# Optimization experiments

Hardware: AMD Instinct MI355X
Metric: run time of the kernel (lower is better)

Reference implementation:

```python
import jax, jax.numpy as jnp
import numpy as np

LAM = 0.01   # sparsity_threshold -> softshrink lambda
EPS = 1e-8

def _ln(x, g, b):
    mu = jnp.mean(x, axis=-1, keepdims=True)
    var = jnp.mean((x - mu) ** 2, axis=-1, keepdims=True)
    return (x - mu) / jnp.sqrt(var + 1e-5) * g + b

def _cmatmul(xr, xi, w, b):
    # x: (B,H,W,nb,i)  w: (2,nb,i,o)  b: (2,nb,o)  -> complex block-diagonal matmul
    o_r = jnp.einsum('bhwni,nio->bhwno', xr, w[0]) - jnp.einsum('bhwni,nio->bhwno', xi, w[1]) + b[0]
    o_i = jnp.einsum('bhwni,nio->bhwno', xi, w[0]) + jnp.einsum('bhwni,nio->bhwno', xr, w[1]) + b[1]
    return o_r, o_i

def _softshrink(v):
    return jnp.where(v > LAM, v - LAM, jnp.where(v < -LAM, v + LAM, 0.0))

def _afno(xn, xp, w1, b1, w2, b2, w3, b3, alpha, H, W):
    # xn: (B,N,C_in) tokens, xp: (B,H,W,hid). layer_i == 0 path, num_blocks == 1.
    B, N, C = xn.shape
    hid = alpha.shape[-1]
    xf = jnp.fft.fft2(xn.reshape(B, H, W, C), axes=(1, 2), norm='ortho')
    xr = xf.real.reshape(B, H, W, 1, C)
    xi = xf.imag.reshape(B, H, W, 1, C)
    o1r, o1i = _cmatmul(xr, xi, w1, b1)           # (B,H,W,1,hid)
    xr = o1r.reshape(B, H, W, hid)
    xi = o1i.reshape(B, H, W, hid)
    pf = jnp.fft.fft2(xp, axes=(1, 2), norm='ortho')
    pr = pf.real.reshape(B, H, W, 1, hid)
    pi = pf.imag.reshape(B, H, W, 1, hid)
    tr, ti = _cmatmul(pr, pi, w3, b3)
    pr = tr.reshape(B, H, W, hid)
    pi = ti.reshape(B, H, W, hid)
    # Pangu-guided frequency modulation (real/imag component form)
    cross_r = pr * xr + pi * xi                   # Re(x_pangu * conj(x))
    mag_o = jnp.sqrt(xr ** 2 + xi ** 2)
    mag_p = jnp.sqrt(pr ** 2 + pi ** 2)
    phi_x = jnp.arctan2(xi, xr)
    phi_p = jnp.arctan2(pi, pr)
    sum_cos = alpha * jnp.cos(phi_x) + (1.0 - alpha) * jnp.cos(phi_p)
    sum_sin = alpha * jnp.sin(phi_x) + (1.0 - alpha) * jnp.sin(phi_p)
    nrm = jnp.sqrt(sum_cos ** 2 + sum_sin ** 2 + EPS)
    out_cos = sum_cos / nrm
    out_sin = sum_sin / nrm
    sim = cross_r / (mag_p * mag_o + EPS)
    soft = jax.nn.softmax(sim, axis=3)
    mag = mag_o * soft
    o1r = jax.nn.relu(mag * out_cos).reshape(B, H, W, 1, hid)
    o1i = jax.nn.relu(mag * out_sin).reshape(B, H, W, 1, hid)
    o2r, o2i = _cmatmul(o1r, o1i, w2, b2)
    o2r = _softshrink(o2r)
    o2i = _softshrink(o2i)
    xc = jax.lax.complex(o2r.reshape(B, H, W, hid), o2i.reshape(B, H, W, hid))
    y = jnp.fft.ifft2(xc, s=(H, W), axes=(1, 2), norm='ortho').real
    return y.reshape(B, N, hid)

def reference(x, x_pangu, z_fft, w1, b1, w2, b2, w3, b3, alpha,
              gamma1, beta1, gamma2, beta2, proj_w, proj_b,
              fc1_w, fc1_b, fc2_w, fc2_b):
    B, C, H, W = x.shape
    tok = x.reshape(B, C, H * W).transpose(0, 2, 1)      # (B,N,C_in)
    xp = x_pangu.transpose(0, 2, 3, 1)                   # (B,H,W,hid)
    residual = tok @ proj_w.T + proj_b                   # C_in != dim -> proj
    f = _afno(_ln(tok, gamma1, beta1), xp, w1, b1, w2, b2, w3, b3, alpha, H, W)
    h = f + residual                                     # double skip
    m = _ln(h, gamma2, beta2)
    m = jax.nn.gelu(m @ fc1_w.T + fc1_b, approximate=False) @ fc2_w.T + fc2_b
    out = m + h
    return out.reshape(B, H, W, -1).transpose(0, 3, 1, 2)

def setup_inputs():
    key = jax.random.key(0)
    ks = jax.random.split(key, 12)
    B, Cin, H, W = 8, 128, 64, 64
    hid, nb, mlp_hid = 256, 1, 2048
    s = 0.02
    return {
        'x': jax.random.normal(ks[0], (B, Cin, H, W), jnp.float32),
        'x_pangu': jax.random.normal(ks[1], (B, hid, H, W), jnp.float32),
        'z_fft': jax.random.normal(ks[2], (B, H, W, hid, 2), jnp.float32),
        'w1': s * jax.random.normal(ks[3], (2, nb, Cin, hid), jnp.float32),
        'b1': s * jax.random.normal(ks[4], (2, nb, hid), jnp.float32),
        'w2': s * jax.random.normal(ks[5], (2, nb, hid, hid), jnp.float32),
        'b2': s * jax.random.normal(ks[6], (2, nb, hid), jnp.float32),
        'w3': s * jax.random.normal(ks[7], (2, nb, hid, hid), jnp.float32),
        'b3': s * jax.random.normal(ks[8], (2, nb, hid), jnp.float32),
        'alpha': jnp.full((1, 1, 1, hid), 0.5, jnp.float32),
        'gamma1': jnp.ones((Cin,), jnp.float32),
        'beta1': jnp.zeros((Cin,), jnp.float32),
        'gamma2': jnp.ones((hid,), jnp.float32),
        'beta2': jnp.zeros((hid,), jnp.float32),
        'proj_w': s * jax.random.normal(ks[9], (hid, Cin), jnp.float32),
        'proj_b': jnp.zeros((hid,), jnp.float32),
        'fc1_w': s * jax.random.normal(ks[10], (mlp_hid, hid), jnp.float32),
        'fc1_b': jnp.zeros((mlp_hid,), jnp.float32),
        'fc2_w': s * jax.random.normal(ks[11], (hid, mlp_hid), jnp.float32),
        'fc2_b': jnp.zeros((hid,), jnp.float32),
    }
```

## Files before the change

kernel.cpp:

```cpp
#include <hip/hip_runtime.h>
#include <hip/hip_bf16.h>
#include <math.h>

#define NBATCH 8
#define HWP 4096
#define NTOK 32768
#define NTOKH 16896
#define CIN 128
#define HID 256
#define MLPH 2048
#define SLOTF 8388608L

typedef unsigned short u16;
typedef __attribute__((ext_vector_type(8))) short bf16x8;
typedef __attribute__((ext_vector_type(4))) float f32x4;
typedef __attribute__((ext_vector_type(8))) unsigned short ushort8_t;
typedef __attribute__((ext_vector_type(2))) unsigned long long u64x2;

__device__ __forceinline__ float bf2f(u16 v) { return __uint_as_float(((unsigned)v) << 16); }
__device__ __forceinline__ u16 f2bf(float f) {
    unsigned u = __float_as_uint(f);
    u = u + 0x7fffu + ((u >> 16) & 1u);
    return (u16)(u >> 16);
}
__device__ __forceinline__ u16 bits2bf(unsigned u) {
    u = u + 0x7fffu + ((u >> 16) & 1u);
    return (u16)(u >> 16);
}
__device__ __forceinline__ unsigned pk_bf16(float lo, float hi) {
    unsigned r;
    asm("v_cvt_pk_bf16_f32 %0, %1, %2" : "=v"(r) : "v"(lo), "v"(hi));
    return r;
}
__device__ __forceinline__ float sshrink(float v) {
    return v > 0.01f ? v - 0.01f : (v < -0.01f ? v + 0.01f : 0.f);
}
__device__ __forceinline__ float fast_gelu(float v) {
    float z = v * fmaf(0.0713548162726f, v * v, 1.59576912161f);
    float t = __builtin_amdgcn_exp2f(z * -1.44269504088896f);
    return v * __builtin_amdgcn_rcpf(1.f + t);
}

__global__ __launch_bounds__(256) void ln1_kernel(const float* __restrict__ x,
    const float* __restrict__ g, const float* __restrict__ be,
    u16* __restrict__ xnb, u16* __restrict__ xb)
{
    __shared__ float xt[CIN][65];
    __shared__ float mu_s[64], rs_s[64];
    int bid = blockIdx.x;
    int b = bid >> 6;
    int t0 = (bid & 63) << 6;
    int tid = threadIdx.x;
    for (int it = 0; it < 32; ++it) {
        int idx = (it << 8) + tid;
        int c = idx >> 6, t = idx & 63;
        xt[c][t] = x[(long)(b * CIN + c) * HWP + t0 + t];
    }
    __syncthreads();
    int tt = tid >> 2, p = tid & 3;
    float s = 0.f, ss = 0.f;
    #pragma unroll
    for (int i = 0; i < 32; ++i) {
        float v = xt[p * 32 + i][tt];
        s += v; ss += v * v;
    }
    s += __shfl_xor(s, 1); ss += __shfl_xor(ss, 1);
    s += __shfl_xor(s, 2); ss += __shfl_xor(ss, 2);
    if (p == 0) {
        float mu = s * (1.f / CIN);
        float var = ss * (1.f / CIN) - mu * mu;
        mu_s[tt] = mu;
        rs_s[tt] = rsqrtf(var + 1e-5f);
    }
    __syncthreads();
    #pragma unroll
    for (int it = 0; it < 16; ++it) {
        int idx = (it << 8) + tid;
        int t = idx >> 6, c2 = (idx & 63) << 1;
        float v0 = (xt[c2][t] - mu_s[t]) * rs_s[t] * g[c2] + be[c2];
        float v1 = (xt[c2 + 1][t] - mu_s[t]) * rs_s[t] * g[c2 + 1] + be[c2 + 1];
        *(unsigned*)&xnb[((long)b * HWP + t0 + t) * CIN + c2] = pk_bf16(v0, v1);
    }
    #pragma unroll
    for (int it = 0; it < 8; ++it) {
        int idx = (it << 8) + tid;
        int t = idx >> 5, c4 = (idx & 31) << 2;
        uint2 pk;
        pk.x = pk_bf16(xt[c4 + 0][t], xt[c4 + 1][t]);
        pk.y = pk_bf16(xt[c4 + 2][t], xt[c4 + 3][t]);
        *(uint2*)&xb[((long)b * HWP + t0 + t) * CIN + c4] = pk;
    }
}

__device__ __forceinline__ void wcvt_body(const float* __restrict__ w, int K,
    u16* __restrict__ out, int idx)
{
    int k = idx >> 8, o = idx & 255;
    float w0 = w[k * 256 + o];
    float w1v = w[K * 256 + k * 256 + o];
    long K2 = 2L * K;
    out[(long)o * K2 + k] = f2bf(w0);
    out[(long)o * K2 + K + k] = f2bf(-w1v);
    out[(long)(256 + o) * K2 + k] = f2bf(w1v);
    out[(long)(256 + o) * K2 + K + k] = f2bf(w0);
}
__device__ __forceinline__ void f2bf_body(const float* __restrict__ in,
    u16* __restrict__ out, int i)
{
    float4 v = *(const float4*)&in[i];
    ushort4 o;
    o.x = f2bf(v.x); o.y = f2bf(v.y); o.z = f2bf(v.z); o.w = f2bf(v.w);
    *(ushort4*)&out[i] = o;
}
__global__ __launch_bounds__(256) void setup_kernel(
    const float* __restrict__ w1, const float* __restrict__ w3,
    const float* __restrict__ w2, const float* __restrict__ fc1w,
    const float* __restrict__ fc2w, const float* __restrict__ pw,
    u16* __restrict__ TWB, u16* __restrict__ W1c, u16* __restrict__ W3c,
    u16* __restrict__ W2c, u16* __restrict__ WB1, u16* __restrict__ WB2,
    u16* __restrict__ PWB)
{
    int bid = blockIdx.x, tid = threadIdx.x;
    if (bid < 64) {
        int idx = bid * 256 + tid;
        int n = idx >> 7, kcol = idx & 127;
        int j = kcol & 63, p = kcol >> 6;
        int np = n & 63, q = n >> 6;
        float th = 6.283185307179586f * (float)((j * np) & 63) / 64.f;
        float sv, cv;
        sincosf(th, &sv, &cv);
        float fw = (q == 0) ? (p == 0 ? cv : sv) : (p == 0 ? -sv : cv);
        float iv = (q == 0) ? (p == 0 ? cv : -sv) : (p == 0 ? sv : cv);
        fw *= 0.125f; iv *= 0.125f;
        u16 fh = f2bf(fw), ih = f2bf(iv);
        TWB[idx] = fh;
        TWB[16384 + idx] = f2bf(fw - bf2f(fh));
        TWB[32768 + idx] = ih;
        TWB[49152 + idx] = f2bf(iv - bf2f(ih));
    } else if (bid < 192) {
        wcvt_body(w1, 128, W1c, (bid - 64) * 256 + tid);
    } else if (bid < 448) {
        wcvt_body(w3, 256, W3c, (bid - 192) * 256 + tid);
    } else if (bid < 704) {
        wcvt_body(w2, 256, W2c, (bid - 448) * 256 + tid);
    } else if (bid < 1216) {
        f2bf_body(fc1w, WB1, ((bid - 704) * 256 + tid) * 4);
    } else if (bid < 1728) {
        f2bf_body(fc2w, WB2, ((bid - 1216) * 256 + tid) * 4);
    } else {
        f2bf_body(pw, PWB, ((bid - 1728) * 256 + tid) * 4);
    }
}

template<int INMODE, int REALOUT, int NT, int USELO>
__global__ __launch_bounds__(256) void dftm_kernel(
    const void* __restrict__ inp, const u16* __restrict__ tw,
    void* __restrict__ outp, const float* __restrict__ addend,
    int nch, long IB, long IK, long IC, long JS, long PS,
    long OB, long OK, long OC, long KS, long PS2, int kmax)
{
    constexpr int K = (INMODE == 1) ? 128 : 64;
    constexpr int AST = (K == 128) ? 136 : 72;
    constexpr int MFR = REALOUT ? 2 : 4;
    __shared__ __align__(16) u16 smem[128 * 136];
    int tid = threadIdx.x;
    int lane = tid & 63;
    int bid = blockIdx.x;
    int b = bid / (64 * nch);
    int rem = bid % (64 * nch);
    int keep = rem / nch;
    int ch = rem % nch;
    long ibase = b * IB + keep * IK + ch * IC;
    long obase = b * OB + keep * OK + ch * OC;

    if (INMODE == 0) {
        const float* inF = (const float*)inp;
        #pragma unroll
        for (int it = 0; it < 8; ++it) {
            int idx = (it << 8) + tid;
            int j = idx >> 5, c4 = (idx & 31) << 2;
            u64x2 v = *(const u64x2*)(inF + ibase + (long)j * JS + c4);
            #pragma unroll
            for (int i = 0; i < 4; ++i) {
                int vv = (i + lane) & 3;
                unsigned long long q = (vv & 2) ? v.y : v.x;
                unsigned fb = (unsigned)(q >> ((vv & 1) << 5));
                smem[(c4 + vv) * AST + j] = bits2bf(fb);
            }
        }
    } else if (INMODE == 1) {
        const u16* inU = (const u16*)inp;
        #pragma unroll
        for (int it = 0; it < 8; ++it) {
            int idx = (it << 8) + tid;
            int run = idx >> 4, c8 = (idx & 15) << 3;
            int j = run >> 1, p = run & 1;
            u64x2 v = *(const u64x2*)(inU + ibase + (long)j * JS + (long)p * PS + c8);
            int col = p * 64 + j;
            #pragma unroll
            for (int i = 0; i < 8; ++i) {
                int vv = (i + lane) & 7;
                unsigned long long q = (vv & 4) ? v.y : v.x;
                u16 val = (u16)(q >> ((vv & 3) << 4));
                smem[(c8 + vv) * AST + col] = val;
            }
        }
    } else if (INMODE == 3) {
        const u16* inU = (const u16*)inp;
        #pragma unroll
        for (int it = 0; it < 4; ++it) {
            int idx = (it << 8) + tid;
            int j = idx >> 4, c8 = (idx & 15) << 3;
            u64x2 v = *(const u64x2*)(inU + ibase + (long)j * JS + c8);
            #pragma unroll
            for (int i = 0; i < 8; ++i) {
                int vv = (i + lane) & 7;
                unsigned long long q = (vv & 4) ? v.y : v.x;
                u16 val = (u16)(q >> ((vv & 3) << 4));
                smem[(c8 + vv) * AST + j] = val;
            }
        }
    } else {
        const float* inF = (const float*)inp;
        #pragma unroll
        for (int it = 0; it < 8; ++it) {
            int idx = (it << 8) + tid;
            int row = idx >> 4, j4 = (idx & 15) << 2;
            u64x2 v = *(const u64x2*)(inF + ibase + (long)row * JS + j4);
            ushort4 o;
            o.x = bits2bf((unsigned)v.x);
            o.y = bits2bf((unsigned)(v.x >> 32));
            o.z = bits2bf((unsigned)v.y);
            o.w = bits2bf((unsigned)(v.y >> 32));
            *(ushort4*)&smem[row * AST + j4] = o;
        }
    }
    __syncthreads();

    int w = tid >> 6;
    int ln15 = lane & 15, kg = lane >> 4;
    int wrow = REALOUT ? (w << 5) : ((w >> 1) << 6);
    int wcol = REALOUT ? 0 : ((w & 1) << 6);
    f32x4 acc[MFR][NT] = {};
    #pragma unroll
    for (int kk = 0; kk < K / 32; ++kk) {
        bf16x8 av[MFR];
        #pragma unroll
        for (int m = 0; m < MFR; ++m)
            av[m] = *(const bf16x8*)&smem[(wrow + m * 16 + ln15) * AST + kk * 32 + kg * 8];
        #pragma unroll
        for (int n = 0; n < NT; ++n) {
            const u16* tb = tw + (wcol + n * 16 + ln15) * 128 + kk * 32 + kg * 8;
            bf16x8 bh = *(const bf16x8*)tb;
            #pragma unroll
            for (int m = 0; m < MFR; ++m)
                acc[m][n] = __builtin_amdgcn_mfma_f32_16x16x32_bf16(av[m], bh, acc[m][n], 0, 0, 0);
            if (USELO) {
                bf16x8 bl = *(const bf16x8*)(tb + 16384);
                #pragma unroll
                for (int m = 0; m < MFR; ++m)
                    acc[m][n] = __builtin_amdgcn_mfma_f32_16x16x32_bf16(av[m], bl, acc[m][n], 0, 0, 0);
            }
        }
    }
    __syncthreads();

    if (REALOUT == 0) {
        #pragma unroll
        for (int m = 0; m < MFR; ++m)
            #pragma unroll
            for (int n = 0; n < NT; ++n) {
                int base = (wcol + n * 16 + ln15) * 136 + wrow + m * 16 + kg * 4;
                uint2 pk;
                pk.x = pk_bf16(acc[m][n][0], acc[m][n][1]);
                pk.y = pk_bf16(acc[m][n][2], acc[m][n][3]);
                *(uint2*)&smem[base] = pk;
            }
        __syncthreads();
        u16* outU = (u16*)outp;
        #pragma unroll
        for (int it = 0; it < 8; ++it) {
            int idx = (it << 8) + tid;
            int n = idx >> 4, c8 = (idx & 15) << 3;
            int k = n & 63, p = n >> 6;
            if (k <= kmax)
                *(ushort8_t*)&outU[obase + (long)k * KS + (long)p * PS2 + c8] =
                    *(const ushort8_t*)&smem[n * 136 + c8];
        }
    } else {
        float* ef = (float*)smem;
        #pragma unroll
        for (int m = 0; m < MFR; ++m)
            #pragma unroll
            for (int n = 0; n < NT; ++n) {
                float4 vv = make_float4(acc[m][n][0], acc[m][n][1], acc[m][n][2], acc[m][n][3]);
                *(float4*)&ef[(n * 16 + ln15) * 132 + wrow + m * 16 + kg * 4] = vv;
            }
        __syncthreads();
        float* outF = (float*)outp;
        #pragma unroll
        for (int it = 0; it < 8; ++it) {
            int idx = (it << 8) + tid;
            int k = idx >> 5, c4 = (idx & 31) << 2;
            long a = obase + (long)k * KS + c4;
            float4 v = *(const float4*)&ef[k * 132 + c4];
            float4 rv = *(const float4*)&addend[a];
            v.x += rv.x; v.y += rv.y; v.z += rv.z; v.w += rv.w;
            *(float4*)&outF[a] = v;
        }
    }
}

__global__ __launch_bounds__(256) void mod_kernel(
    const u16* __restrict__ x1, const u16* __restrict__ p3,
    const float* __restrict__ alpha, u16* __restrict__ a2)
{
    int tid = threadIdx.x;
    int lane = tid & 63;
    int wv = tid >> 6;
    int tp = blockIdx.x * 4 + wv;
    int b = tp / 2112;
    int r = tp - b * 2112;
    int kh = r >> 6, kw = r & 63;
    long ibase = (long)tp * 512 + lane * 4;
    ushort4 xr4 = *(const ushort4*)&x1[ibase];
    ushort4 xi4 = *(const ushort4*)&x1[ibase + 256];
    ushort4 pr4 = *(const ushort4*)&p3[ibase];
    ushort4 pi4 = *(const ushort4*)&p3[ibase + 256];
    float4 al4 = *(const float4*)&alpha[lane * 4];
    u16 xru[4] = {xr4.x, xr4.y, xr4.z, xr4.w};
    u16 xiu[4] = {xi4.x, xi4.y, xi4.z, xi4.w};
    u16 pru[4] = {pr4.x, pr4.y, pr4.z, pr4.w};
    u16 piu[4] = {pi4.x, pi4.y, pi4.z, pi4.w};
    float alv[4] = {al4.x, al4.y, al4.z, al4.w};
    float mo[4], oc[4], os[4], sim[4];
    #pragma unroll
    for (int q = 0; q < 4; ++q) {
        float xr = bf2f(xru[q]), xi = bf2f(xiu[q]);
        float pr = bf2f(pru[q]), pi = bf2f(piu[q]);
        float al = alv[q];
        float m = __builtin_amdgcn_sqrtf(xr * xr + xi * xi);
        float mp = __builtin_amdgcn_sqrtf(pr * pr + pi * pi);
        float cx, sx, cp, sp;
        if (m > 0.f) { float rr = __builtin_amdgcn_rcpf(m); cx = xr * rr; sx = xi * rr; }
        else { cx = 1.f; sx = 0.f; }
        if (mp > 0.f) { float rr = __builtin_amdgcn_rcpf(mp); cp = pr * rr; sp = pi * rr; }
        else { cp = 1.f; sp = 0.f; }
        float sc = al * cx + (1.f - al) * cp;
        float ssn = al * sx + (1.f - al) * sp;
        float rn = __builtin_amdgcn_rsqf(sc * sc + ssn * ssn + 1e-8f);
        mo[q] = m;
        oc[q] = sc * rn;
        os[q] = ssn * rn;
        float cross = pr * xr + pi * xi;
        sim[q] = cross * __builtin_amdgcn_rcpf(mp * m + 1e-8f);
    }
    float mv = fmaxf(fmaxf(sim[0], sim[1]), fmaxf(sim[2], sim[3]));
    #pragma unroll
    for (int off = 1; off < 64; off <<= 1) mv = fmaxf(mv, __shfl_xor(mv, off));
    float e[4];
    float sum = 0.f;
    #pragma unroll
    for (int q = 0; q < 4; ++q) {
        e[q] = __builtin_amdgcn_exp2f((sim[q] - mv) * 1.44269504088896f);
        sum += e[q];
    }
    #pragma unroll
    for (int off = 1; off < 64; off <<= 1) sum += __shfl_xor(sum, off);
    float rs = __builtin_amdgcn_rcpf(sum);
    float orf[4], ipf[4], imf[4];
    #pragma unroll
    for (int q = 0; q < 4; ++q) {
        float mag = mo[q] * e[q] * rs;
        orf[q] = fmaxf(mag * oc[q], 0.f);
        ipf[q] = fmaxf(mag * os[q], 0.f);
        imf[q] = fmaxf(-mag * os[q], 0.f);
    }
    uint2 o_r, o_ip, o_im;
    o_r.x = pk_bf16(orf[0], orf[1]);  o_r.y = pk_bf16(orf[2], orf[3]);
    o_ip.x = pk_bf16(ipf[0], ipf[1]); o_ip.y = pk_bf16(ipf[2], ipf[3]);
    o_im.x = pk_bf16(imf[0], imf[1]); o_im.y = pk_bf16(imf[2], imf[3]);
    long pbase = ((long)b * 4096 + kh * 64 + kw) * 512 + lane * 4;
    *(uint2*)&a2[pbase] = o_r;
    *(uint2*)&a2[pbase + 256] = o_ip;
    if (kh >= 1 && kh <= 31) {
        long mbase = ((long)b * 4096 + (64 - kh) * 64 + ((64 - kw) & 63)) * 512 + lane * 4;
        *(uint2*)&a2[mbase] = o_r;
        *(uint2*)&a2[mbase + 256] = o_im;
    }
}

__global__ __launch_bounds__(256) void ln2_kernel(const float* __restrict__ h,
    const float* __restrict__ g, const float* __restrict__ be, u16* __restrict__ m)
{
    int t = blockIdx.x, c = threadIdx.x;
    float v = h[(long)t * HID + c];
    float s = v, ss = v * v;
    #pragma unroll
    for (int off = 1; off < 64; off <<= 1) { s += __shfl_xor(s, off); ss += __shfl_xor(ss, off); }
    __shared__ float r1[4], r2[4];
    int wid = c >> 6;
    if ((c & 63) == 0) { r1[wid] = s; r2[wid] = ss; }
    __syncthreads();
    s = r1[0] + r1[1] + r1[2] + r1[3];
    ss = r2[0] + r2[1] + r2[2] + r2[3];
    float mu = s * (1.f / HID);
    float var = ss * (1.f / HID) - mu * mu;
    float rstd = rsqrtf(var + 1e-5f);
    m[(long)t * HID + c] = f2bf((v - mu) * rstd * g[c] + be[c]);
}

template<int EPI, int BK>
__global__ __launch_bounds__(256) void gemm_mfma_kernel(
    const u16* __restrict__ A, const u16* __restrict__ Bw,
    const float* __restrict__ bias, const float* __restrict__ hbuf,
    void* __restrict__ outp, int M, int N, int K)
{
    constexpr bool SWAP = (EPI == 0 || EPI == 2 || EPI == 4);
    __shared__ __align__(16) char smem[(EPI == 1 || EPI == 5) ? (128 * 132 * 4) : (128 * 136 * 2)];
    u16* ldsA = (u16*)smem;
    u16* ldsB = (u16*)(smem + 128 * BK * 2);
    int tid = threadIdx.x;
    int nbn = N >> 7;
    int cpx = (int)gridDim.x >> 3;
    int bid = ((int)blockIdx.x & 7) * cpx + ((int)blockIdx.x >> 3);
    int bRow = (bid / nbn) << 7;
    int bCol = (bid % nbn) << 7;
    int lane = tid & 63;
    int w = tid >> 6;
    int wr = (w >> 1) << 6;
    int wc = (w & 1) << 6;
    int ln15 = lane & 15;
    int kg = lane >> 4;

    f32x4 acc[4][4] = {};

    constexpr int GR = BK / 8;
    int srow = tid / GR;
    int sg = tid % GR;
    int gsg = sg ^ (srow & 7);
    const u16* gA = A + (long)(bRow + srow) * K + gsg * 8;
    const u16* gB = Bw + (long)(bCol + srow) * K + gsg * 8;
    u16* lA = ldsA + srow * BK + sg * 8;
    u16* lB = ldsB + srow * BK + sg * 8;
    constexpr int RPR = 256 / GR;
    constexpr int NCH = 128 / RPR;

    for (int k0 = 0; k0 < K; k0 += BK) {
        __syncthreads();
        #pragma unroll
        for (int c = 0; c < NCH; ++c) {
            __builtin_amdgcn_global_load_lds(
                (const __attribute__((address_space(1))) void*)(gA + (long)c * RPR * K + k0),
                (__attribute__((address_space(3))) void*)(lA + c * RPR * BK), 16, 0, 0);
            __builtin_amdgcn_global_load_lds(
                (const __attribute__((address_space(1))) void*)(gB + (long)c * RPR * K + k0),
                (__attribute__((address_space(3))) void*)(lB + c * RPR * BK), 16, 0, 0);
        }
        __syncthreads();
        #pragma unroll
        for (int kk = 0; kk < BK; kk += 32) {
            int gbase = (kk >> 3) + kg;
            bf16x8 av[4], bv[4];
            #pragma unroll
            for (int m = 0; m < 4; ++m) {
                int row = wr + m * 16 + ln15;
                av[m] = *(const bf16x8*)(ldsA + row * BK + ((gbase ^ (row & 7)) << 3));
            }
            #pragma unroll
            for (int n = 0; n < 4; ++n) {
                int row = wc + n * 16 + ln15;
                bv[n] = *(const bf16x8*)(ldsB + row * BK + ((gbase ^ (row & 7)) << 3));
            }
            #pragma unroll
            for (int m = 0; m < 4; ++m)
                #pragma unroll
                for (int n = 0; n < 4; ++n) {
                    if (SWAP)
                        acc[m][n] = __builtin_amdgcn_mfma_f32_16x16x32_bf16(bv[n], av[m], acc[m][n], 0, 0, 0);
                    else
                        acc[m][n] = __builtin_amdgcn_mfma_f32_16x16x32_bf16(av[m], bv[n], acc[m][n], 0, 0, 0);
                }
        }
    }
    __syncthreads();

    if (EPI == 0 || EPI == 2 || EPI == 4) {
        u16* lds2 = (u16*)smem;
        #pragma unroll
        for (int n = 0; n < 4; ++n) {
            float4 bn4 = *(const float4*)&bias[bCol + wc + n * 16 + kg * 4];
            #pragma unroll
            for (int m = 0; m < 4; ++m) {
                float v0 = acc[m][n][0] + bn4.x;
                float v1 = acc[m][n][1] + bn4.y;
                float v2 = acc[m][n][2] + bn4.z;
                float v3 = acc[m][n][3] + bn4.w;
                if (EPI == 0) { v0 = fast_gelu(v0); v1 = fast_gelu(v1); v2 = fast_gelu(v2); v3 = fast_gelu(v3); }
                if (EPI == 4) { v0 = sshrink(v0); v1 = sshrink(v1); v2 = sshrink(v2); v3 = sshrink(v3); }
                uint2 pk;
                pk.x = pk_bf16(v0, v1);
                pk.y = pk_bf16(v2, v3);
                int tokenLocal = wr + m * 16 + ln15;
                int nLocal = wc + n * 16 + kg * 4;
                *(uint2*)&lds2[tokenLocal * 136 + nLocal] = pk;
            }
        }
        __syncthreads();
        u16* O = (u16*)outp;
        #pragma unroll
        for (int it = 0; it < 8; ++it) {
            int idx = (it << 8) + tid;
            int row = idx >> 4, c8 = (idx & 15) << 3;
            *(ushort8_t*)&O[(long)(bRow + row) * N + bCol + c8] = *(const ushort8_t*)&lds2[row * 136 + c8];
        }
    } else if (EPI == 5) {
        float* ldsf = (float*)smem;
        float bn[4];
        #pragma unroll
        for (int n = 0; n < 4; ++n) bn[n] = bias[bCol + wc + n * 16 + ln15];
        #pragma unroll
        for (int m = 0; m < 4; ++m)
            #pragma unroll
            for (int n = 0; n < 4; ++n) {
                int col = wc + n * 16 + ln15;
                #pragma unroll
                for (int r = 0; r < 4; ++r) {
                    int row = wr + m * 16 + kg * 4 + r;
                    ldsf[row * 132 + col] = acc[m][n][r] + bn[n];
                }
            }
        __syncthreads();
        float* O = (float*)outp;
        #pragma unroll
        for (int it = 0; it < 16; ++it) {
            int idx = (it << 8) + tid;
            int row = idx >> 5, c4 = (idx & 31) << 2;
            *(float4*)&O[(long)(bRow + row) * N + bCol + c4] = *(const float4*)&ldsf[row * 132 + c4];
        }
    } else {
        float* ldsf = (float*)smem;
        float bn[4];
        #pragma unroll
        for (int n = 0; n < 4; ++n) bn[n] = bias[bCol + wc + n * 16 + ln15];
        #pragma unroll
        for (int m = 0; m < 4; ++m)
            #pragma unroll
            for (int n = 0; n < 4; ++n) {
                int col = wc + n * 16 + ln15;
                float4 vv;
                #pragma unroll
                for (int r = 0; r < 4; ++r) {
                    int row = wr + m * 16 + kg * 4 + r;
                    float v = acc[m][n][r] + bn[n] + hbuf[(long)(bRow + row) * HID + bCol + col];
                    ((float*)&vv)[r] = v;
                }
                *(float4*)&ldsf[col * 132 + wr + m * 16 + kg * 4] = vv;
            }
        __syncthreads();
        float* O = (float*)outp;
        int b = bRow >> 12;
        int s0 = bRow & 4095;
        #pragma unroll
        for (int it = 0; it < 16; ++it) {
            int idx = (it << 8) + tid;
            int oc = idx >> 5, r4 = (idx & 31) << 2;
            *(float4*)&O[((long)(b * HID + bCol + oc)) * HWP + s0 + r4] = *(const float4*)&ldsf[oc * 132 + r4];
        }
    }
}

extern "C" void kernel_launch(void* const* d_in, const int* in_sizes, int n_in,
                              void* d_out, int out_size, void* d_ws, size_t ws_size,
                              hipStream_t stream)
{
    (void)in_sizes; (void)n_in; (void)out_size; (void)ws_size;
    const float* x     = (const float*)d_in[0];
    const float* xp    = (const float*)d_in[1];
    const float* w1    = (const float*)d_in[3];
    const float* b1    = (const float*)d_in[4];
    const float* w2    = (const float*)d_in[5];
    const float* b2    = (const float*)d_in[6];
    const float* w3    = (const float*)d_in[7];
    const float* b3    = (const float*)d_in[8];
    const float* alpha = (const float*)d_in[9];
    const float* g1    = (const float*)d_in[10];
    const float* be1   = (const float*)d_in[11];
    const float* g2    = (const float*)d_in[12];
    const float* be2   = (const float*)d_in[13];
    const float* pw    = (const float*)d_in[14];
    const float* pb    = (const float*)d_in[15];
    const float* fc1w  = (const float*)d_in[16];
    const float* fc1b  = (const float*)d_in[17];
    const float* fc2w  = (const float*)d_in[18];
    const float* fc2b  = (const float*)d_in[19];
    float* out = (float*)d_out;

    float* ws = (float*)d_ws;
    float* S0 = ws + 0 * SLOTF;
    float* S1 = ws + 1 * SLOTF;
    float* S2 = ws + 2 * SLOTF;
    float* S3 = ws + 3 * SLOTF;
    float* S4 = ws + 4 * SLOTF;
    float* S5 = ws + 5 * SLOTF;
    float* S6 = ws + 6 * SLOTF;

    float* RES  = S0;
    u16*   XNB  = (u16*)S1;
    u16*   M1x  = (u16*)S2;
    u16*   XF   = (u16*)S3;
    u16*   X1   = (u16*)S4;
    u16*   M1p  = (u16*)S2;
    u16*   PF   = (u16*)S3;
    u16*   P3   = (u16*)S5;
    u16*   A2   = (u16*)S2;
    u16*   O2b  = (u16*)S3;
    u16*   M2   = (u16*)S2;
    float* Hb   = S6;
    u16*   Mb16 = (u16*)S1;
    u16*   HIDB = (u16*)S2;

    u16* TWB  = (u16*)(S1 + SLOTF / 2);
    u16* TW_F = TWB;
    u16* TW_I = TWB + 32768;
    u16* W1c  = TWB + 65536;
    u16* W3c  = W1c + 131072;
    u16* W2c  = W3c + 262144;
    u16* WB1  = W2c + 262144;
    u16* WB2  = WB1 + 524288;
    u16* PWB  = WB2 + 524288;
    u16* XB   = TWB + 2097152;

    dim3 blk(256);

    setup_kernel<<<1760, blk, 0, stream>>>(w1, w3, w2, fc1w, fc2w, pw,
        TWB, W1c, W3c, W2c, WB1, WB2, PWB);

    ln1_kernel<<<512, blk, 0, stream>>>(x, g1, be1, XNB, XB);
    gemm_mfma_kernel<5, 128><<<512, blk, 0, stream>>>(XB, PWB, pb, nullptr,
        (void*)RES, NTOK, HID, CIN);

    dftm_kernel<3, 0, 4, 0><<<512, blk, 0, stream>>>(XNB, TW_F, M1x, nullptr,
        1, 524288L, 8192L, 0L, 128L, 0L, 1048576L, 16384L, 0L, 128L, 8192L, 63);
    dftm_kernel<1, 0, 3, 0><<<512, blk, 0, stream>>>(M1x, TW_F, XF, nullptr,
        1, 1048576L, 128L, 0L, 16384L, 8192L, 540672L, 256L, 0L, 16384L, 128L, 32);
    gemm_mfma_kernel<2, 64><<<528, blk, 0, stream>>>(XF, W1c, b1, nullptr,
        (void*)X1, NTOKH, 512, 256);

    dftm_kernel<2, 0, 4, 0><<<1024, blk, 0, stream>>>(xp, TW_F, M1p, nullptr,
        2, 1048576L, 64L, 524288L, 4096L, 0L, 2097152L, 32768L, 128L, 256L, 16384L, 63);
    dftm_kernel<1, 0, 3, 0><<<1024, blk, 0, stream>>>(M1p, TW_F, PF, nullptr,
        2, 2097152L, 256L, 128L, 32768L, 16384L, 1081344L, 512L, 128L, 32768L, 256L, 32);
    gemm_mfma_kernel<2, 64><<<528, blk, 0, stream>>>(PF, W3c, b3, nullptr,
        (void*)P3, NTOKH, 512, 512);

    mod_kernel<<<4224, blk, 0, stream>>>(X1, P3, alpha, A2);
    gemm_mfma_kernel<4, 64><<<1024, blk, 0, stream>>>(A2, W2c, b2, nullptr,
        (void*)O2b, NTOK, 512, 512);

    dftm_kernel<1, 0, 4, 0><<<1024, blk, 0, stream>>>(O2b, TW_I, M2, nullptr,
        2, 2097152L, 512L, 128L, 32768L, 256L, 2097152L, 256L, 128L, 32768L, 16384L, 63);
    dftm_kernel<1, 1, 4, 1><<<1024, blk, 0, stream>>>(M2, TW_I, Hb, RES,
        2, 2097152L, 32768L, 128L, 256L, 16384L, 1048576L, 16384L, 128L, 256L, 0L, 63);

    ln2_kernel<<<32768, blk, 0, stream>>>(Hb, g2, be2, Mb16);
    gemm_mfma_kernel<0, 64><<<4096, blk, 0, stream>>>(Mb16, WB1, fc1b, nullptr,
        (void*)HIDB, NTOK, MLPH, HID);
    gemm_mfma_kernel<1, 128><<<512, blk, 0, stream>>>(HIDB, WB2, fc2b, Hb,
        (void*)out, NTOK, HID, MLPH);
}
```

Baseline: 332.4 us.

## Double-buffer LDS tiles in MFMA GEMM to overlap global loads with compute

The GEMM kernel now uses two 64-wide K tiles in LDS and issues the global-to-LDS loads for the next tile before computing on the current one, with one barrier per iteration instead of two. BK is fixed at 64 for all GEMMs, including those that previously used 128. This aims to hide global load latency behind MFMA work. In exchange, LDS use per block grows to 64 KB, which may lower occupancy. Relying on a single barrier per iteration without an explicit vmcnt wait also risks the async LDS loads not being complete when the tile is read.

```diff
diff --git a/kernel.cpp b/kernel.cpp
--- a/kernel.cpp
+++ b/kernel.cpp
@@ -410,16 +410,14 @@
     m[(long)t * HID + c] = f2bf((v - mu) * rstd * g[c] + be[c]);
 }
 
-template<int EPI, int BK>
+template<int EPI>
 __global__ __launch_bounds__(256) void gemm_mfma_kernel(
     const u16* __restrict__ A, const u16* __restrict__ Bw,
     const float* __restrict__ bias, const float* __restrict__ hbuf,
     void* __restrict__ outp, int M, int N, int K)
 {
     constexpr bool SWAP = (EPI == 0 || EPI == 2 || EPI == 4);
-    __shared__ __align__(16) char smem[(EPI == 1 || EPI == 5) ? (128 * 132 * 4) : (128 * 136 * 2)];
-    u16* ldsA = (u16*)smem;
-    u16* ldsB = (u16*)(smem + 128 * BK * 2);
+    __shared__ __align__(16) char smem[(EPI == 1 || EPI == 5) ? (128 * 132 * 4) : 65536];
     int tid = threadIdx.x;
     int nbn = N >> 7;
     int cpx = (int)gridDim.x >> 3;
@@ -435,42 +433,60 @@
 
     f32x4 acc[4][4] = {};
 
-    constexpr int GR = BK / 8;
-    int srow = tid / GR;
-    int sg = tid % GR;
+    int srow = tid >> 3;
+    int sg = tid & 7;
     int gsg = sg ^ (srow & 7);
     const u16* gA = A + (long)(bRow + srow) * K + gsg * 8;
     const u16* gB = Bw + (long)(bCol + srow) * K + gsg * 8;
-    u16* lA = ldsA + srow * BK + sg * 8;
-    u16* lB = ldsB + srow * BK + sg * 8;
-    constexpr int RPR = 256 / GR;
-    constexpr int NCH = 128 / RPR;
-
-    for (int k0 = 0; k0 < K; k0 += BK) {
+
+    int nt = K >> 6;
+
+    {
+        u16* lA = (u16*)smem + srow * 64 + sg * 8;
+        u16* lB = (u16*)(smem + 16384) + srow * 64 + sg * 8;
+        #pragma unroll
+        for (int c = 0; c < 4; ++c) {
+            __builtin_amdgcn_global_load_lds(
+                (const __attribute__((address_space(1))) void*)(gA + (long)c * 32 * K),
+                (__attribute__((address_space(3))) void*)(lA + c * 32 * 64), 16, 0, 0);
+            __builtin_amdgcn_global_load_lds(
+                (const __attribute__((address_space(1))) void*)(gB + (long)c * 32 * K),
+                (__attribute__((address_space(3))) void*)(lB + c * 32 * 64), 16, 0, 0);
+        }
+    }
+
+    int cur = 0;
+    for (int t = 0; t < nt; ++t) {
         __syncthreads();
-        #pragma unroll
-        for (int c = 0; c < NCH; ++c) {
-            __builtin_amdgcn_global_load_lds(
-                (const __attribute__((address_space(1))) void*)(gA + (long)c * RPR * K + k0),
-                (__attribute__((address_space(3))) void*)(lA + c * RPR * BK), 16, 0, 0);
-            __builtin_amdgcn_global_load_lds(
-                (const __attribute__((address_space(1))) void*)(gB + (long)c * RPR * K + k0),
-                (__attribute__((address_space(3))) void*)(lB + c * RPR * BK), 16, 0, 0);
-        }
-        __syncthreads();
-        #pragma unroll
-        for (int kk = 0; kk < BK; kk += 32) {
+        if (t + 1 < nt) {
+            int k0 = (t + 1) << 6;
+            u16* lA = (u16*)(smem + (cur ^ 1) * 32768) + srow * 64 + sg * 8;
+            u16* lB = (u16*)(smem + (cur ^ 1) * 32768 + 16384) + srow * 64 + sg * 8;
+            #pragma unroll
+            for (int c = 0; c < 4; ++c) {
+                __builtin_amdgcn_global_load_lds(
+                    (const __attribute__((address_space(1))) void*)(gA + (long)c * 32 * K + k0),
+                    (__attribute__((address_space(3))) void*)(lA + c * 32 * 64), 16, 0, 0);
+                __builtin_amdgcn_global_load_lds(
+                    (const __attribute__((address_space(1))) void*)(gB + (long)c * 32 * K + k0),
+                    (__attribute__((address_space(3))) void*)(lB + c * 32 * 64), 16, 0, 0);
+            }
+        }
+        u16* ldsA = (u16*)(smem + cur * 32768);
+        u16* ldsB = (u16*)(smem + cur * 32768 + 16384);
+        #pragma unroll
+        for (int kk = 0; kk < 64; kk += 32) {
             int gbase = (kk >> 3) + kg;
             bf16x8 av[4], bv[4];
             #pragma unroll
             for (int m = 0; m < 4; ++m) {
                 int row = wr + m * 16 + ln15;
-                av[m] = *(const bf16x8*)(ldsA + row * BK + ((gbase ^ (row & 7)) << 3));
+                av[m] = *(const bf16x8*)(ldsA + row * 64 + ((gbase ^ (row & 7)) << 3));
             }
             #pragma unroll
             for (int n = 0; n < 4; ++n) {
                 int row = wc + n * 16 + ln15;
-                bv[n] = *(const bf16x8*)(ldsB + row * BK + ((gbase ^ (row & 7)) << 3));
+                bv[n] = *(const bf16x8*)(ldsB + row * 64 + ((gbase ^ (row & 7)) << 3));
             }
             #pragma unroll
             for (int m = 0; m < 4; ++m)
@@ -482,6 +498,7 @@
                         acc[m][n] = __builtin_amdgcn_mfma_f32_16x16x32_bf16(av[m], bv[n], acc[m][n], 0, 0, 0);
                 }
         }
+        cur ^= 1;
     }
     __syncthreads();
 
@@ -637,25 +654,25 @@
         TWB, W1c, W3c, W2c, WB1, WB2, PWB);
 
     ln1_kernel<<<512, blk, 0, stream>>>(x, g1, be1, XNB, XB);
-    gemm_mfma_kernel<5, 128><<<512, blk, 0, stream>>>(XB, PWB, pb, nullptr,
+    gemm_mfma_kernel<5><<<512, blk, 0, stream>>>(XB, PWB, pb, nullptr,
         (void*)RES, NTOK, HID, CIN);
 
     dftm_kernel<3, 0, 4, 0><<<512, blk, 0, stream>>>(XNB, TW_F, M1x, nullptr,
         1, 524288L, 8192L, 0L, 128L, 0L, 1048576L, 16384L, 0L, 128L, 8192L, 63);
     dftm_kernel<1, 0, 3, 0><<<512, blk, 0, stream>>>(M1x, TW_F, XF, nullptr,
         1, 1048576L, 128L, 0L, 16384L, 8192L, 540672L, 256L, 0L, 16384L, 128L, 32);
-    gemm_mfma_kernel<2, 64><<<528, blk, 0, stream>>>(XF, W1c, b1, nullptr,
+    gemm_mfma_kernel<2><<<528, blk, 0, stream>>>(XF, W1c, b1, nullptr,
         (void*)X1, NTOKH, 512, 256);
 
     dftm_kernel<2, 0, 4, 0><<<1024, blk, 0, stream>>>(xp, TW_F, M1p, nullptr,
         2, 1048576L, 64L, 524288L, 4096L, 0L, 2097152L, 32768L, 128L, 256L, 16384L, 63);
     dftm_kernel<1, 0, 3, 0><<<1024, blk, 0, stream>>>(M1p, TW_F, PF, nullptr,
         2, 2097152L, 256L, 128L, 32768L, 16384L, 1081344L, 512L, 128L, 32768L, 256L, 32);
-    gemm_mfma_kernel<2, 64><<<528, blk, 0, stream>>>(PF, W3c, b3, nullptr,
+    gemm_mfma_kernel<2><<<528, blk, 0, stream>>>(PF, W3c, b3, nullptr,
         (void*)P3, NTOKH, 512, 512);
 
     mod_kernel<<<4224, blk, 0, stream>>>(X1, P3, alpha, A2);
-    gemm_mfma_kernel<4, 64><<<1024, blk, 0, stream>>>(A2, W2c, b2, nullptr,
+    gemm_mfma_kernel<4><<<1024, blk, 0, stream>>>(A2, W2c, b2, nullptr,
         (void*)O2b, NTOK, 512, 512);
 
     dftm_kernel<1, 0, 4, 0><<<1024, blk, 0, stream>>>(O2b, TW_I, M2, nullptr,
@@ -664,8 +681,8 @@
         2, 2097152L, 32768L, 128L, 256L, 16384L, 1048576L, 16384L, 128L, 256L, 0L, 63);
 
     ln2_kernel<<<32768, blk, 0, stream>>>(Hb, g2, be2, Mb16);
-    gemm_mfma_kernel<0, 64><<<4096, blk, 0, stream>>>(Mb16, WB1, fc1b, nullptr,
+    gemm_mfma_kernel<0><<<4096, blk, 0, stream>>>(Mb16, WB1, fc1b, nullptr,
         (void*)HIDB, NTOK, MLPH, HID);
-    gemm_mfma_kernel<1, 128><<<512, blk, 0, stream>>>(HIDB, WB2, fc2b, Hb,
+    gemm_mfma_kernel<1><<<512, blk, 0, stream>>>(HIDB, WB2, fc2b, Hb,
         (void*)out, NTOK, HID, MLPH);
 }
```

Result: no change. 336.5 us (+1.2%).

## Store MLP hidden activations and fc2 weights in FP8 and run fc2 with FP8 MFMA

Applied to the files above, without the earlier changes.

The fc1 GEMM epilogue now applies GELU and packs its output to FP8 (E4M3) instead of bf16, which halves the size of the 32768x2048 hidden tensor that is written and then read back. The fc2 weights are converted to FP8 during setup. A new dedicated fc2 kernel uses global_load_lds with an XOR-swizzled LDS layout and the 16x16x32 FP8 MFMA, followed by the same bias, residual and transposed-store epilogue as before. The gain is less memory traffic and higher MFMA throughput for the K=2048 GEMM, at the cost of reduced precision with no scaling factors, which risks exceeding the accuracy tolerance.

```diff
diff --git a/kernel.cpp b/kernel.cpp
--- a/kernel.cpp
+++ b/kernel.cpp
@@ -12,6 +12,7 @@
 #define SLOTF 8388608L
 
 typedef unsigned short u16;
+typedef unsigned char u8;
 typedef __attribute__((ext_vector_type(8))) short bf16x8;
 typedef __attribute__((ext_vector_type(4))) float f32x4;
 typedef __attribute__((ext_vector_type(8))) unsigned short ushort8_t;
@@ -31,6 +32,11 @@
     unsigned r;
     asm("v_cvt_pk_bf16_f32 %0, %1, %2" : "=v"(r) : "v"(lo), "v"(hi));
     return r;
+}
+__device__ __forceinline__ unsigned pk4_fp8(float v0, float v1, float v2, float v3) {
+    int r = __builtin_amdgcn_cvt_pk_fp8_f32(v0, v1, 0, false);
+    r = __builtin_amdgcn_cvt_pk_fp8_f32(v2, v3, r, true);
+    return (unsigned)r;
 }
 __device__ __forceinline__ float sshrink(float v) {
     return v > 0.01f ? v - 0.01f : (v < -0.01f ? v + 0.01f : 0.f);
@@ -117,7 +123,7 @@
     const float* __restrict__ w2, const float* __restrict__ fc1w,
     const float* __restrict__ fc2w, const float* __restrict__ pw,
     u16* __restrict__ TWB, u16* __restrict__ W1c, u16* __restrict__ W3c,
-    u16* __restrict__ W2c, u16* __restrict__ WB1, u16* __restrict__ WB2,
+    u16* __restrict__ W2c, u16* __restrict__ WB1, unsigned* __restrict__ WB2F,
     u16* __restrict__ PWB)
 {
     int bid = blockIdx.x, tid = threadIdx.x;
@@ -146,7 +152,9 @@
     } else if (bid < 1216) {
         f2bf_body(fc1w, WB1, ((bid - 704) * 256 + tid) * 4);
     } else if (bid < 1728) {
-        f2bf_body(fc2w, WB2, ((bid - 1216) * 256 + tid) * 4);
+        int i = ((bid - 1216) * 256 + tid) * 4;
+        float4 v = *(const float4*)&fc2w[i];
+        WB2F[i >> 2] = pk4_fp8(v.x, v.y, v.z, v.w);
     } else {
         f2bf_body(pw, PWB, ((bid - 1728) * 256 + tid) * 4);
     }
@@ -416,8 +424,8 @@
     const float* __restrict__ bias, const float* __restrict__ hbuf,
     void* __restrict__ outp, int M, int N, int K)
 {
-    constexpr bool SWAP = (EPI == 0 || EPI == 2 || EPI == 4);
-    __shared__ __align__(16) char smem[(EPI == 1 || EPI == 5) ? (128 * 132 * 4) : (128 * 136 * 2)];
+    constexpr bool SWAP = (EPI == 0 || EPI == 2 || EPI == 4 || EPI == 6);
+    __shared__ __align__(16) char smem[(EPI == 5) ? (128 * 132 * 4) : (128 * 136 * 2)];
     u16* ldsA = (u16*)smem;
     u16* ldsB = (u16*)(smem + 128 * BK * 2);
     int tid = threadIdx.x;
@@ -514,7 +522,32 @@
             int row = idx >> 4, c8 = (idx & 15) << 3;
             *(ushort8_t*)&O[(long)(bRow + row) * N + bCol + c8] = *(const ushort8_t*)&lds2[row * 136 + c8];
         }
-    } else if (EPI == 5) {
+    } else if (EPI == 6) {
+        unsigned* lds2 = (unsigned*)smem;
+        #pragma unroll
+        for (int n = 0; n < 4; ++n) {
+            float4 bn4 = *(const float4*)&bias[bCol + wc + n * 16 + kg * 4];
+            #pragma unroll
+            for (int m = 0; m < 4; ++m) {
+                float v0 = fast_gelu(acc[m][n][0] + bn4.x);
+                float v1 = fast_gelu(acc[m][n][1] + bn4.y);
+                float v2 = fast_gelu(acc[m][n][2] + bn4.z);
+                float v3 = fast_gelu(acc[m][n][3] + bn4.w);
+                int tokenLocal = wr + m * 16 + ln15;
+                int nLocal = wc + n * 16 + kg * 4;
+                lds2[tokenLocal * 36 + (nLocal >> 2)] = pk4_fp8(v0, v1, v2, v3);
+            }
+        }
+        __syncthreads();
+        u8* O = (u8*)outp;
+        #pragma unroll
+        for (int it = 0; it < 4; ++it) {
+            int idx = (it << 8) + tid;
+            int row = idx >> 3, u = idx & 7;
+            uint4 vv = *(const uint4*)&lds2[row * 36 + u * 4];
+            *(uint4*)&O[(long)(bRow + row) * (long)N + bCol + u * 16] = vv;
+        }
+    } else {
         float* ldsf = (float*)smem;
         float bn[4];
         #pragma unroll
@@ -538,35 +571,100 @@
             int row = idx >> 5, c4 = (idx & 31) << 2;
             *(float4*)&O[(long)(bRow + row) * N + bCol + c4] = *(const float4*)&ldsf[row * 132 + c4];
         }
-    } else {
-        float* ldsf = (float*)smem;
-        float bn[4];
-        #pragma unroll
-        for (int n = 0; n < 4; ++n) bn[n] = bias[bCol + wc + n * 16 + ln15];
-        #pragma unroll
-        for (int m = 0; m < 4; ++m)
+    }
+}
+
+__global__ __launch_bounds__(256) void mlp2_fp8_kernel(
+    const u8* __restrict__ A, const u8* __restrict__ Bw,
+    const float* __restrict__ bias, const float* __restrict__ hbuf,
+    float* __restrict__ out)
+{
+    __shared__ __align__(16) char smem[128 * 132 * 4];
+    u8* ldsA = (u8*)smem;
+    u8* ldsB = (u8*)(smem + 8192);
+    int tid = threadIdx.x;
+    int cpx = (int)gridDim.x >> 3;
+    int bid = ((int)blockIdx.x & 7) * cpx + ((int)blockIdx.x >> 3);
+    int bRow = (bid >> 1) << 7;
+    int bCol = (bid & 1) << 7;
+    int lane = tid & 63;
+    int w = tid >> 6;
+    int wr = (w >> 1) << 6;
+    int wc = (w & 1) << 6;
+    int ln15 = lane & 15;
+    int kg = lane >> 4;
+
+    f32x4 acc[4][4] = {};
+
+    int srow = tid >> 2;
+    int sg = tid & 3;
+    int gsg = sg ^ (srow & 3);
+    const u8* gA = A + (long)(bRow + srow) * MLPH + gsg * 16;
+    const u8* gB = Bw + (long)(bCol + srow) * MLPH + gsg * 16;
+    u8* lA = ldsA + srow * 64 + sg * 16;
+    u8* lB = ldsB + srow * 64 + sg * 16;
+
+    for (int k0 = 0; k0 < MLPH; k0 += 64) {
+        __syncthreads();
+        #pragma unroll
+        for (int c = 0; c < 2; ++c) {
+            __builtin_amdgcn_global_load_lds(
+                (const __attribute__((address_space(1))) void*)(gA + (long)c * 64 * MLPH + k0),
+                (__attribute__((address_space(3))) void*)(lA + c * 64 * 64), 16, 0, 0);
+            __builtin_amdgcn_global_load_lds(
+                (const __attribute__((address_space(1))) void*)(gB + (long)c * 64 * MLPH + k0),
+                (__attribute__((address_space(3))) void*)(lB + c * 64 * 64), 16, 0, 0);
+        }
+        __syncthreads();
+        #pragma unroll
+        for (int kk = 0; kk < 64; kk += 32) {
+            int boff = kk + kg * 8;
+            long long av[4], bv[4];
+            #pragma unroll
+            for (int m = 0; m < 4; ++m) {
+                int row = wr + m * 16 + ln15;
+                av[m] = *(const long long*)(ldsA + row * 64 + (((boff >> 4) ^ (row & 3)) << 4) + (boff & 15));
+            }
             #pragma unroll
             for (int n = 0; n < 4; ++n) {
-                int col = wc + n * 16 + ln15;
-                float4 vv;
+                int row = wc + n * 16 + ln15;
+                bv[n] = *(const long long*)(ldsB + row * 64 + (((boff >> 4) ^ (row & 3)) << 4) + (boff & 15));
+            }
+            #pragma unroll
+            for (int m = 0; m < 4; ++m)
                 #pragma unroll
-                for (int r = 0; r < 4; ++r) {
-                    int row = wr + m * 16 + kg * 4 + r;
-                    float v = acc[m][n][r] + bn[n] + hbuf[(long)(bRow + row) * HID + bCol + col];
-                    ((float*)&vv)[r] = v;
-                }
-                *(float4*)&ldsf[col * 132 + wr + m * 16 + kg * 4] = vv;
-            }
-        __syncthreads();
-        float* O = (float*)outp;
-        int b = bRow >> 12;
-        int s0 = bRow & 4095;
-        #pragma unroll
-        for (int it = 0; it < 16; ++it) {
-            int idx = (it << 8) + tid;
-            int oc = idx >> 5, r4 = (idx & 31) << 2;
-            *(float4*)&O[((long)(b * HID + bCol + oc)) * HWP + s0 + r4] = *(const float4*)&ldsf[oc * 132 + r4];
-        }
+                for (int n = 0; n < 4; ++n)
+                    acc[m][n] = __builtin_amdgcn_mfma_f32_16x16x32_fp8_fp8(av[m], bv[n], acc[m][n], 0, 0, 0);
+        }
+    }
+    __syncthreads();
+
+    float* ldsf = (float*)smem;
+    float bn[4];
+    #pragma unroll
+    for (int n = 0; n < 4; ++n) bn[n] = bias[bCol + wc + n * 16 + ln15];
+    #pragma unroll
+    for (int m = 0; m < 4; ++m)
+        #pragma unroll
+        for (int n = 0; n < 4; ++n) {
+            int col = wc + n * 16 + ln15;
+            float4 vv;
+            #pragma unroll
+            for (int r = 0; r < 4; ++r) {
+                int row = wr + m * 16 + kg * 4 + r;
+                float v = acc[m][n][r] + bn[n] + hbuf[(long)(bRow + row) * HID + bCol + col];
+                ((float*)&vv)[r] = v;
+            }
+            *(float4*)&ldsf[col * 132 + wr + m * 16 + kg * 4] = vv;
+        }
+    __syncthreads();
+    int b = bRow >> 12;
+    int s0 = bRow & 4095;
+    #pragma unroll
+    for (int it = 0; it < 16; ++it) {
+        int idx = (it << 8) + tid;
+        int oc = idx >> 5, r4 = (idx & 31) << 2;
+        *(float4*)&out[((long)(b * HID + bCol + oc)) * HWP + s0 + r4] = *(const float4*)&ldsf[oc * 132 + r4];
     }
 }
 
@@ -618,7 +716,7 @@
     u16*   M2   = (u16*)S2;
     float* Hb   = S6;
     u16*   Mb16 = (u16*)S1;
-    u16*   HIDB = (u16*)S2;
+    u8*    HIDF8 = (u8*)S2;
 
     u16* TWB  = (u16*)(S1 + SLOTF / 2);
     u16* TW_F = TWB;
@@ -627,14 +725,14 @@
     u16* W3c  = W1c + 131072;
     u16* W2c  = W3c + 262144;
     u16* WB1  = W2c + 262144;
-    u16* WB2  = WB1 + 524288;
-    u16* PWB  = WB2 + 524288;
+    unsigned* WB2F = (unsigned*)(WB1 + 524288);
+    u16* PWB  = WB1 + 524288 + 524288;
     u16* XB   = TWB + 2097152;
 
     dim3 blk(256);
 
     setup_kernel<<<1760, blk, 0, stream>>>(w1, w3, w2, fc1w, fc2w, pw,
-        TWB, W1c, W3c, W2c, WB1, WB2, PWB);
+        TWB, W1c, W3c, W2c, WB1, WB2F, PWB);
 
     ln1_kernel<<<512, blk, 0, stream>>>(x, g1, be1, XNB, XB);
     gemm_mfma_kernel<5, 128><<<512, blk, 0, stream>>>(XB, PWB, pb, nullptr,
@@ -664,8 +762,7 @@
         2, 2097152L, 32768L, 128L, 256L, 16384L, 1048576L, 16384L, 128L, 256L, 0L, 63);
 
     ln2_kernel<<<32768, blk, 0, stream>>>(Hb, g2, be2, Mb16);
-    gemm_mfma_kernel<0, 64><<<4096, blk, 0, stream>>>(Mb16, WB1, fc1b, nullptr,
-        (void*)HIDB, NTOK, MLPH, HID);
-    gemm_mfma_kernel<1, 128><<<512, blk, 0, stream>>>(HIDB, WB2, fc2b, Hb,
-        (void*)out, NTOK, HID, MLPH);
-}
+    gemm_mfma_kernel<6, 64><<<4096, blk, 0, stream>>>(Mb16, WB1, fc1b, nullptr,
+        (void*)HIDF8, NTOK, MLPH, HID);
+    mlp2_fp8_kernel<<<512, blk, 0, stream>>>(HIDF8, (const u8*)WB2F, fc2b, Hb, out);
+}
```

New measurement: 331.1 us. No clear change (-0.4%).
